# Kernel optimization log

Measured on AMD Instinct MI355X. Metric: run time of the kernel, lower is better.

## Reference

```python
import jax, jax.numpy as jnp
import numpy as np

BATCH, SEQ, IN_DIM = 512, 512, 64
H1, H2, OUT = 100, 100, 1


def setup_inputs() -> dict:
    key = jax.random.key(0)
    ks = jax.random.split(key, 7)
    s = lambda fan_in: 1.0 / np.sqrt(fan_in)
    return {
        "x":   jax.random.normal(ks[0], (BATCH, SEQ, IN_DIM), dtype=jnp.float32),
        "W1x": jax.random.normal(ks[1], (IN_DIM, H1), dtype=jnp.float32) * s(IN_DIM),
        "W1h": jax.random.normal(ks[2], (H1, H1), dtype=jnp.float32) * s(H1),
        "b1":  jnp.zeros((H1,), dtype=jnp.float32),
        "W2x": jax.random.normal(ks[3], (H1, H2), dtype=jnp.float32) * s(H1),
        "W2h": jax.random.normal(ks[4], (H2, H2), dtype=jnp.float32) * s(H2),
        "b2":  jnp.zeros((H2,), dtype=jnp.float32),
        "Wo":  jax.random.normal(ks[5], (H2, OUT), dtype=jnp.float32) * s(H2),
        "bo":  jnp.zeros((OUT,), dtype=jnp.float32),
    }


def reference(x, W1x, W1h, b1, W2x, W2h, b2, Wo, bo):
    # Two stacked SimpleRNN layers (tanh), fused in a single scan over time.
    # Keras SimpleRNN: h_t = tanh(x_t @ Wx + h_{t-1} @ Wh + b)
    B = x.shape[0]
    h1_0 = jnp.zeros((B, W1h.shape[0]), dtype=x.dtype)
    h2_0 = jnp.zeros((B, W2h.shape[0]), dtype=x.dtype)

    def step(carry, x_t):
        h1, h2 = carry
        h1 = jnp.tanh(x_t @ W1x + h1 @ W1h + b1)   # [B, H1]
        h2 = jnp.tanh(h1 @ W2x + h2 @ W2h + b2)    # [B, H2]
        return (h1, h2), None

    xs = jnp.swapaxes(x, 0, 1)                      # [T, B, D]
    (h1_T, h2_T), _ = jax.lax.scan(step, (h1_0, h2_0), xs)
    out = h2_T @ Wo + bo                            # [B, 1]
    return out, h1_T, h2_T
```

## Files before the change

### kernel.cpp

```cpp
#include <hip/hip_runtime.h>
#include <math.h>

#define T      512
#define NBATCH 512
#define IN_DIM 64
#define H      100
#define KCAT   208
#define NCHUNK 52
#define CPT    13

__device__ __forceinline__ float fast_tanh(float a) {
    float e = __expf(2.0f * a);
    return 1.0f - 2.0f / (e + 1.0f);
}

__device__ __forceinline__ float wval(const float* __restrict__ WA,
                                      const float* __restrict__ WB,
                                      int kvA, int R, int col) {
    if (R < 104) {
        int rr = (R < kvA) ? R : 0;
        float v = WA[rr * H + col];
        return (R < kvA) ? v : 0.f;
    }
    int rb = R - 104;
    int rr = (rb < H) ? rb : 0;
    float v = WB[rr * H + col];
    return (rb < H) ? v : 0.f;
}

__device__ __forceinline__ float4 wload4(const float* __restrict__ WA,
                                         const float* __restrict__ WB,
                                         int kvA, int R0, int col) {
    return make_float4(wval(WA, WB, kvA, R0 + 0, col),
                       wval(WA, WB, kvA, R0 + 1, col),
                       wval(WA, WB, kvA, R0 + 2, col),
                       wval(WA, WB, kvA, R0 + 3, col));
}


#define CHUNKS(X) X(0) X(1) X(2) X(3) X(4) X(5) X(6) X(7) X(8) X(9) X(10) X(11) X(12)

#define WDECL(C) float4 wq##C##_0, wq##C##_1, wq##C##_2, wq##C##_3;

#define WLOADC(C) { const int R0_ = 16 * (C) + 4 * s;            \
    wq##C##_0 = wload4(WpA, WpB, kvA, R0_, c0);                  \
    wq##C##_1 = wload4(WpA, WpB, kvA, R0_, c1);                  \
    wq##C##_2 = wload4(WpA, WpB, kvA, R0_, c2);                  \
    wq##C##_3 = wload4(WpA, WpB, kvA, R0_, c3); }

#define STEP(C) { float4 v_ = pin_[4 * (C) + s];                                  \
    a0 = fmaf(v_.x, wq##C##_0.x, a0); a1 = fmaf(v_.x, wq##C##_1.x, a1);           \
    a2 = fmaf(v_.x, wq##C##_2.x, a2); a3 = fmaf(v_.x, wq##C##_3.x, a3);           \
    a0 = fmaf(v_.y, wq##C##_0.y, a0); a1 = fmaf(v_.y, wq##C##_1.y, a1);           \
    a2 = fmaf(v_.y, wq##C##_2.y, a2); a3 = fmaf(v_.y, wq##C##_3.y, a3);           \
    a0 = fmaf(v_.z, wq##C##_0.z, a0); a1 = fmaf(v_.z, wq##C##_1.z, a1);           \
    a2 = fmaf(v_.z, wq##C##_2.z, a2); a3 = fmaf(v_.z, wq##C##_3.z, a3);           \
    a0 = fmaf(v_.w, wq##C##_0.w, a0); a1 = fmaf(v_.w, wq##C##_1.w, a1);           \
    a2 = fmaf(v_.w, wq##C##_2.w, a2); a3 = fmaf(v_.w, wq##C##_3.w, a3); }

#define DOT(pin, hv) {                                           \
    const float4* pin_ = (pin);                                  \
    float a0 = 0.f, a1 = 0.f, a2 = 0.f, a3 = 0.f;                \
    CHUNKS(STEP)                                                 \
    a0 += __shfl_xor(a0, 1); a1 += __shfl_xor(a1, 1);            \
    a2 += __shfl_xor(a2, 1); a3 += __shfl_xor(a3, 1);            \
    a0 += __shfl_xor(a0, 2); a1 += __shfl_xor(a1, 2);            \
    a2 += __shfl_xor(a2, 2); a3 += __shfl_xor(a3, 2);            \
    float t_ = (s == 0) ? a0 : (s == 1) ? a1 : (s == 2) ? a2 : a3; \
    hv = fast_tanh(t_ + bj); }

__global__ __launch_bounds__(256, 2)
void drnn_kernel(const float* __restrict__ x,
                 const float* __restrict__ W1x, const float* __restrict__ W1h,
                 const float* __restrict__ b1,
                 const float* __restrict__ W2x, const float* __restrict__ W2h,
                 const float* __restrict__ b2,
                 const float* __restrict__ Wo,  const float* __restrict__ bo,
                 float* __restrict__ out)
{
    __shared__ __align__(16) float in1[2][KCAT];
    __shared__ __align__(16) float in2[2][KCAT];

    const int tid = threadIdx.x;
    const int b   = blockIdx.x;
    const float* __restrict__ xrow = x + (size_t)b * T * IN_DIM;

    for (int k = tid; k < 2 * KCAT; k += 256) {
        (&in1[0][0])[k] = 0.f;
        (&in2[0][0])[k] = 0.f;
    }
    if (tid < IN_DIM) in1[0][tid] = xrow[tid];

    const bool isL1 = (tid < 128);
    const int  idx  = tid & 127;
    const int  g    = idx >> 2;
    const int  s    = idx & 3;
    const int  j    = 4 * g;
    const bool stok = (g < 25);
    const int  c0 = (j + 0 < H) ? j + 0 : H - 1;
    const int  c1 = (j + 1 < H) ? j + 1 : H - 1;
    const int  c2 = (j + 2 < H) ? j + 2 : H - 1;
    const int  c3 = (j + 3 < H) ? j + 3 : H - 1;
    const int  cs = (j + s < H) ? j + s : H - 1;

    const float* __restrict__ WpA = isL1 ? W1x : W2x;
    const float* __restrict__ WpB = isL1 ? W1h : W2h;
    const int kvA = isL1 ? IN_DIM : H;
    const float bj = (isL1 ? b1 : b2)[cs];

    CHUNKS(WDECL)
    CHUNKS(WLOADC)

    const float4* pe = (const float4*)(isL1 ? in1[0] : in2[0]);
    const float4* po = (const float4*)(isL1 ? in1[1] : in2[1]);
    float* w1a_e = &in1[1][104 + cs];
    float* w1b_e = &in2[1][cs];
    float* w2_e  = &in2[1][104 + cs];
    float* w1a_o = &in1[0][104 + cs];
    float* w1b_o = &in2[0][cs];
    float* w2_o  = &in2[0][104 + cs];

    float xr0 = 0.f, xr1 = 0.f;
    if (tid < 64) {
        xr0 = xrow[1 * IN_DIM + tid];
        xr1 = xrow[2 * IN_DIM + tid];
    }

    __syncthreads();

    #pragma unroll 1
    for (int i = 0; i < T; i += 2) {
        {
            float hv;
            DOT(pe, hv)
            if (isL1) {
                if (stok) { *w1a_e = hv; *w1b_e = hv; }
            } else if (stok && i > 0) {
                *w2_e = hv;
            }
            if (tid < 64) {
                in1[1][tid] = xr0;
                xr0 = xr1;
                if (i + 3 < T) xr1 = xrow[(size_t)(i + 3) * IN_DIM + tid];
            }
        }
        __syncthreads();
        {
            float hv;
            DOT(po, hv)
            if (isL1) {
                if (stok) { *w1a_o = hv; *w1b_o = hv; }
            } else if (stok) {
                *w2_o = hv;
            }
            if (tid < 64) {
                in1[0][tid] = xr0;
                xr0 = xr1;
                if (i + 4 < T) xr1 = xrow[(size_t)(i + 4) * IN_DIM + tid];
            }
        }
        __syncthreads();
    }

    if (!isL1) {
        float hv;
        DOT(pe, hv)
        if (stok) *w2_e = hv;
    }
    __syncthreads();

    if (tid < H)
        out[NBATCH + (size_t)b * H + tid] = in1[0][104 + tid];
    if (tid < H)
        out[NBATCH + (size_t)NBATCH * H + (size_t)b * H + tid] = in2[1][104 + tid];

    if (tid < 64) {
        float v = in2[1][104 + tid] * Wo[tid];
        if (tid + 64 < H) v += in2[1][104 + 64 + tid] * Wo[tid + 64];
        #pragma unroll
        for (int off = 32; off >= 1; off >>= 1) v += __shfl_down(v, off);
        if (tid == 0) out[b] = v + bo[0];
    }
}

extern "C" void kernel_launch(void* const* d_in, const int* in_sizes, int n_in,
                              void* d_out, int out_size, void* d_ws, size_t ws_size,
                              hipStream_t stream) {
    const float* x   = (const float*)d_in[0];
    const float* W1x = (const float*)d_in[1];
    const float* W1h = (const float*)d_in[2];
    const float* b1  = (const float*)d_in[3];
    const float* W2x = (const float*)d_in[4];
    const float* W2h = (const float*)d_in[5];
    const float* b2  = (const float*)d_in[6];
    const float* Wo  = (const float*)d_in[7];
    const float* bo  = (const float*)d_in[8];
    float* out = (float*)d_out;

    drnn_kernel<<<NBATCH, 256, 0, stream>>>(x, W1x, W1h, b1, W2x, W2h, b2,
                                            Wo, bo, out);
}
```

Measured before the change: 540.6 us.

## Split each dot product across 8 lanes with DPP reduction and 512-thread blocks

Doubles the block to 512 threads so each output group of 4 hidden units is computed by 8 lanes instead of 4, which halves the per-thread K-loop length and weight registers on the serial recurrence path. The shared-memory concatenation buffer is packed densely (x|h1 and h1|h2 without padding gaps). The cross-lane reduction uses DPP row operations instead of shuffles, and a dedicated wave prefetches x. It adds more threads per block and a third reduction stage, and may lower occupancy per CU.

```diff
diff --git a/kernel.cpp b/kernel.cpp
--- a/kernel.cpp
+++ b/kernel.cpp
@@ -5,71 +5,74 @@
 #define NBATCH 512
 #define IN_DIM 64
 #define H      100
-#define KCAT   208
-#define NCHUNK 52
-#define CPT    13
+#define KP     208
+#define PBYTES 832
 
 __device__ __forceinline__ float fast_tanh(float a) {
     float e = __expf(2.0f * a);
     return 1.0f - 2.0f / (e + 1.0f);
 }
 
+#define DPP_ADD(v, ctrl) ((v) + __int_as_float(__builtin_amdgcn_update_dpp( \
+        0, __float_as_int(v), (ctrl), 0xF, 0xF, true)))
+#define RED8(a) { (a) = DPP_ADD((a), 0xB1);    \
+                  (a) = DPP_ADD((a), 0x4E);    \
+                  (a) = DPP_ADD((a), 0x128);   }
+
 __device__ __forceinline__ float wval(const float* __restrict__ WA,
                                       const float* __restrict__ WB,
-                                      int kvA, int R, int col) {
-    if (R < 104) {
-        int rr = (R < kvA) ? R : 0;
-        float v = WA[rr * H + col];
-        return (R < kvA) ? v : 0.f;
-    }
-    int rb = R - 104;
-    int rr = (rb < H) ? rb : 0;
-    float v = WB[rr * H + col];
-    return (rb < H) ? v : 0.f;
+                                      int kA, int R, int col) {
+    if (R < kA) return WA[R * H + col];
+    int rr = R - kA;
+    return (rr < H) ? WB[rr * H + col] : 0.f;
 }
 
 __device__ __forceinline__ float4 wload4(const float* __restrict__ WA,
                                          const float* __restrict__ WB,
-                                         int kvA, int R0, int col) {
-    return make_float4(wval(WA, WB, kvA, R0 + 0, col),
-                       wval(WA, WB, kvA, R0 + 1, col),
-                       wval(WA, WB, kvA, R0 + 2, col),
-                       wval(WA, WB, kvA, R0 + 3, col));
-}
-
-
-#define CHUNKS(X) X(0) X(1) X(2) X(3) X(4) X(5) X(6) X(7) X(8) X(9) X(10) X(11) X(12)
-
-#define WDECL(C) float4 wq##C##_0, wq##C##_1, wq##C##_2, wq##C##_3;
-
-#define WLOADC(C) { const int R0_ = 16 * (C) + 4 * s;            \
-    wq##C##_0 = wload4(WpA, WpB, kvA, R0_, c0);                  \
-    wq##C##_1 = wload4(WpA, WpB, kvA, R0_, c1);                  \
-    wq##C##_2 = wload4(WpA, WpB, kvA, R0_, c2);                  \
-    wq##C##_3 = wload4(WpA, WpB, kvA, R0_, c3); }
-
-#define STEP(C) { float4 v_ = pin_[4 * (C) + s];                                  \
-    a0 = fmaf(v_.x, wq##C##_0.x, a0); a1 = fmaf(v_.x, wq##C##_1.x, a1);           \
-    a2 = fmaf(v_.x, wq##C##_2.x, a2); a3 = fmaf(v_.x, wq##C##_3.x, a3);           \
-    a0 = fmaf(v_.y, wq##C##_0.y, a0); a1 = fmaf(v_.y, wq##C##_1.y, a1);           \
-    a2 = fmaf(v_.y, wq##C##_2.y, a2); a3 = fmaf(v_.y, wq##C##_3.y, a3);           \
-    a0 = fmaf(v_.z, wq##C##_0.z, a0); a1 = fmaf(v_.z, wq##C##_1.z, a1);           \
-    a2 = fmaf(v_.z, wq##C##_2.z, a2); a3 = fmaf(v_.z, wq##C##_3.z, a3);           \
-    a0 = fmaf(v_.w, wq##C##_0.w, a0); a1 = fmaf(v_.w, wq##C##_1.w, a1);           \
-    a2 = fmaf(v_.w, wq##C##_2.w, a2); a3 = fmaf(v_.w, wq##C##_3.w, a3); }
-
-#define DOT(pin, hv) {                                           \
-    const float4* pin_ = (pin);                                  \
-    float a0 = 0.f, a1 = 0.f, a2 = 0.f, a3 = 0.f;                \
-    CHUNKS(STEP)                                                 \
-    a0 += __shfl_xor(a0, 1); a1 += __shfl_xor(a1, 1);            \
-    a2 += __shfl_xor(a2, 1); a3 += __shfl_xor(a3, 1);            \
-    a0 += __shfl_xor(a0, 2); a1 += __shfl_xor(a1, 2);            \
-    a2 += __shfl_xor(a2, 2); a3 += __shfl_xor(a3, 2);            \
-    float t_ = (s == 0) ? a0 : (s == 1) ? a1 : (s == 2) ? a2 : a3; \
-    hv = fast_tanh(t_ + bj); }
-
-__global__ __launch_bounds__(256, 2)
+                                         int kA, int R0, int col) {
+    return make_float4(wval(WA, WB, kA, R0 + 0, col),
+                       wval(WA, WB, kA, R0 + 1, col),
+                       wval(WA, WB, kA, R0 + 2, col),
+                       wval(WA, WB, kA, R0 + 3, col));
+}
+
+
+#define RNDS(X) X(0) X(1) X(2) X(3) X(4) X(5)
+
+#define WDECL(R) float4 w##R##_0 = {0,0,0,0}, w##R##_1 = {0,0,0,0}, \
+                        w##R##_2 = {0,0,0,0}, w##R##_3 = {0,0,0,0};
+
+#define WLOAD(R) { const int r0_ = 32 * (R) + 4 * s;   \
+    w##R##_0 = wload4(WA, WB, kA, r0_, j + 0);         \
+    w##R##_1 = wload4(WA, WB, kA, r0_, j + 1);         \
+    w##R##_2 = wload4(WA, WB, kA, r0_, j + 2);         \
+    w##R##_3 = wload4(WA, WB, kA, r0_, j + 3); }
+
+#define FSTEP(R, P) { const float4 v_ = *(const float4*)(rb + (P) + 128 * (R)); \
+    a0 = fmaf(v_.x, w##R##_0.x, a0); a1 = fmaf(v_.x, w##R##_1.x, a1);           \
+    a2 = fmaf(v_.x, w##R##_2.x, a2); a3 = fmaf(v_.x, w##R##_3.x, a3);           \
+    a0 = fmaf(v_.y, w##R##_0.y, a0); a1 = fmaf(v_.y, w##R##_1.y, a1);           \
+    a2 = fmaf(v_.y, w##R##_2.y, a2); a3 = fmaf(v_.y, w##R##_3.y, a3);           \
+    a0 = fmaf(v_.z, w##R##_0.z, a0); a1 = fmaf(v_.z, w##R##_1.z, a1);           \
+    a2 = fmaf(v_.z, w##R##_2.z, a2); a3 = fmaf(v_.z, w##R##_3.z, a3);           \
+    a0 = fmaf(v_.w, w##R##_0.w, a0); a1 = fmaf(v_.w, w##R##_1.w, a1);           \
+    a2 = fmaf(v_.w, w##R##_2.w, a2); a3 = fmaf(v_.w, w##R##_3.w, a3); }
+
+#define DOT(P, hv) {                                                 \
+    float a0 = 0.f, a1 = 0.f, a2 = 0.f, a3 = 0.f;                    \
+    FSTEP(0, P) FSTEP(1, P) FSTEP(2, P)                              \
+    FSTEP(3, P) FSTEP(4, P) FSTEP(5, P)                              \
+    { const float2 v_ = *(const float2*)(tb + (P));                  \
+      a0 = fmaf(v_.x, wt0.x, a0); a1 = fmaf(v_.x, wt1.x, a1);        \
+      a2 = fmaf(v_.x, wt2.x, a2); a3 = fmaf(v_.x, wt3.x, a3);        \
+      a0 = fmaf(v_.y, wt0.y, a0); a1 = fmaf(v_.y, wt1.y, a1);        \
+      a2 = fmaf(v_.y, wt2.y, a2); a3 = fmaf(v_.y, wt3.y, a3); }      \
+    RED8(a0) RED8(a1) RED8(a2) RED8(a3)                              \
+    const float t01_ = (s & 1) ? a1 : a0;                            \
+    const float t23_ = (s & 1) ? a3 : a2;                            \
+    hv = fast_tanh(((s & 2) ? t23_ : t01_) + bj); }
+
+__global__ __launch_bounds__(512, 4)
 void drnn_kernel(const float* __restrict__ x,
                  const float* __restrict__ W1x, const float* __restrict__ W1h,
                  const float* __restrict__ b1,
@@ -78,105 +81,102 @@
                  const float* __restrict__ Wo,  const float* __restrict__ bo,
                  float* __restrict__ out)
 {
-    __shared__ __align__(16) float in1[2][KCAT];
-    __shared__ __align__(16) float in2[2][KCAT];
-
-    const int tid = threadIdx.x;
-    const int b   = blockIdx.x;
+    __shared__ __align__(16) float in1[2][KP];
+    __shared__ __align__(16) float in2[2][KP];
+
+    const int tid  = threadIdx.x;
+    const int b    = blockIdx.x;
+    const int lane = tid & 63;
+    const int wv   = tid >> 6;
+    const int s    = (lane & 3) | ((lane >> 1) & 4);
+    const int gw   = ((lane >> 2) & 1) | ((lane >> 3) & 6);
+    const int gg   = wv * 8 + gw;
+    const bool active = (gg < 50);
+    const bool isL1   = (gg < 25);
+    const bool isXL   = (wv == 7);
+
     const float* __restrict__ xrow = x + (size_t)b * T * IN_DIM;
 
-    for (int k = tid; k < 2 * KCAT; k += 256) {
+    for (int k = tid; k < 2 * KP; k += 512) {
         (&in1[0][0])[k] = 0.f;
         (&in2[0][0])[k] = 0.f;
     }
     if (tid < IN_DIM) in1[0][tid] = xrow[tid];
 
-    const bool isL1 = (tid < 128);
-    const int  idx  = tid & 127;
-    const int  g    = idx >> 2;
-    const int  s    = idx & 3;
-    const int  j    = 4 * g;
-    const bool stok = (g < 25);
-    const int  c0 = (j + 0 < H) ? j + 0 : H - 1;
-    const int  c1 = (j + 1 < H) ? j + 1 : H - 1;
-    const int  c2 = (j + 2 < H) ? j + 2 : H - 1;
-    const int  c3 = (j + 3 < H) ? j + 3 : H - 1;
-    const int  cs = (j + s < H) ? j + s : H - 1;
-
-    const float* __restrict__ WpA = isL1 ? W1x : W2x;
-    const float* __restrict__ WpB = isL1 ? W1h : W2h;
-    const int kvA = isL1 ? IN_DIM : H;
-    const float bj = (isL1 ? b1 : b2)[cs];
-
-    CHUNKS(WDECL)
-    CHUNKS(WLOADC)
-
-    const float4* pe = (const float4*)(isL1 ? in1[0] : in2[0]);
-    const float4* po = (const float4*)(isL1 ? in1[1] : in2[1]);
-    float* w1a_e = &in1[1][104 + cs];
-    float* w1b_e = &in2[1][cs];
-    float* w2_e  = &in2[1][104 + cs];
-    float* w1a_o = &in1[0][104 + cs];
-    float* w1b_o = &in2[0][cs];
-    float* w2_o  = &in2[0][104 + cs];
-
+    const float* __restrict__ WA = isL1 ? W1x : W2x;
+    const float* __restrict__ WB = isL1 ? W1h : W2h;
+    const int kA = isL1 ? IN_DIM : H;
+    const int gl = isL1 ? gg : gg - 25;
+    const int nl = (gl >= 0 && gl < 25) ? gl : 0;
+    const int j  = 4 * nl;
+    const int n  = j + (s & 3);
+    const float bj = active ? (isL1 ? b1 : b2)[n] : 0.f;
+
+    RNDS(WDECL)
+    float2 wt0 = {0,0}, wt1 = {0,0}, wt2 = {0,0}, wt3 = {0,0};
+    if (active) {
+        RNDS(WLOAD)
+        const int rt = 192 + 2 * s;
+        wt0 = make_float2(wval(WA,WB,kA,rt,j+0), wval(WA,WB,kA,rt+1,j+0));
+        wt1 = make_float2(wval(WA,WB,kA,rt,j+1), wval(WA,WB,kA,rt+1,j+1));
+        wt2 = make_float2(wval(WA,WB,kA,rt,j+2), wval(WA,WB,kA,rt+1,j+2));
+        wt3 = make_float2(wval(WA,WB,kA,rt,j+3), wval(WA,WB,kA,rt+1,j+3));
+    }
+
+    const char* lb = (const char*)(isL1 ? &in1[0][0] : &in2[0][0]);
+    const char* rb = lb + 16 * s;
+    const char* tb = lb + 768 + 8 * s;
+
+    char* st;
+    if (isL1) st = (char*)((s < 4) ? &in1[0][64 + n] : &in2[0][n]);
+    else      st = (char*)&in2[0][100 + n];
+    const bool dost = active && (isL1 || s < 4);
+
+    char* xw = (char*)&in1[0][lane];
     float xr0 = 0.f, xr1 = 0.f;
-    if (tid < 64) {
-        xr0 = xrow[1 * IN_DIM + tid];
-        xr1 = xrow[2 * IN_DIM + tid];
+    if (isXL) {
+        xr0 = xrow[IN_DIM + lane];
+        xr1 = xrow[2 * IN_DIM + lane];
     }
 
     __syncthreads();
 
     #pragma unroll 1
     for (int i = 0; i < T; i += 2) {
-        {
-            float hv;
-            DOT(pe, hv)
-            if (isL1) {
-                if (stok) { *w1a_e = hv; *w1b_e = hv; }
-            } else if (stok && i > 0) {
-                *w2_e = hv;
-            }
-            if (tid < 64) {
-                in1[1][tid] = xr0;
-                xr0 = xr1;
-                if (i + 3 < T) xr1 = xrow[(size_t)(i + 3) * IN_DIM + tid];
-            }
+        if (active) {
+            float hv; DOT(0, hv)
+            if (dost && (isL1 || i > 0)) *(float*)(st + PBYTES) = hv;
+        } else if (isXL) {
+            *(float*)(xw + PBYTES) = xr0;
+            xr0 = xr1;
+            if (i + 3 < T) xr1 = xrow[(size_t)(i + 3) * IN_DIM + lane];
         }
         __syncthreads();
-        {
-            float hv;
-            DOT(po, hv)
-            if (isL1) {
-                if (stok) { *w1a_o = hv; *w1b_o = hv; }
-            } else if (stok) {
-                *w2_o = hv;
-            }
-            if (tid < 64) {
-                in1[0][tid] = xr0;
-                xr0 = xr1;
-                if (i + 4 < T) xr1 = xrow[(size_t)(i + 4) * IN_DIM + tid];
-            }
+        if (active) {
+            float hv; DOT(PBYTES, hv)
+            if (dost) *(float*)st = hv;
+        } else if (isXL) {
+            *(float*)xw = xr0;
+            xr0 = xr1;
+            if (i + 4 < T) xr1 = xrow[(size_t)(i + 4) * IN_DIM + lane];
         }
         __syncthreads();
     }
 
-    if (!isL1) {
-        float hv;
-        DOT(pe, hv)
-        if (stok) *w2_e = hv;
+    if (active && !isL1) {
+        float hv; DOT(0, hv)
+        if (s < 4) *(float*)(st + PBYTES) = hv;
     }
     __syncthreads();
 
     if (tid < H)
-        out[NBATCH + (size_t)b * H + tid] = in1[0][104 + tid];
+        out[NBATCH + (size_t)b * H + tid] = in1[0][64 + tid];
     if (tid < H)
-        out[NBATCH + (size_t)NBATCH * H + (size_t)b * H + tid] = in2[1][104 + tid];
+        out[NBATCH + (size_t)NBATCH * H + (size_t)b * H + tid] = in2[1][100 + tid];
 
     if (tid < 64) {
-        float v = in2[1][104 + tid] * Wo[tid];
-        if (tid + 64 < H) v += in2[1][104 + 64 + tid] * Wo[tid + 64];
+        float v = in2[1][100 + tid] * Wo[tid];
+        if (tid + 64 < H) v += in2[1][100 + 64 + tid] * Wo[tid + 64];
         #pragma unroll
         for (int off = 32; off >= 1; off >>= 1) v += __shfl_down(v, off);
         if (tid == 0) out[b] = v + bo[0];
@@ -197,6 +197,6 @@
     const float* bo  = (const float*)d_in[8];
     float* out = (float*)d_out;
 
-    drnn_kernel<<<NBATCH, 256, 0, stream>>>(x, W1x, W1h, b1, W2x, W2h, b2,
+    drnn_kernel<<<NBATCH, 512, 0, stream>>>(x, W1x, W1h, b1, W2x, W2h, b2,
                                             Wo, bo, out);
 }
```

Result: faster. 512.4 us (-5.2%).
